# Kernel optimization log

Hardware: AMD Instinct MI355X
Metric: run time of the kernel (lower is better)

The kernel has to match this reference:

```python
import jax, jax.numpy as jnp
import numpy as np

B, N, C = 8, 1024, 768
H = 12
HD = C // H  # 64


def setup_inputs() -> dict:
    key = jax.random.key(0)
    k1, k2, k3, k4 = jax.random.split(key, 4)
    x = jax.random.normal(k1, (B, N, C), dtype=jnp.float32)
    # nn.Linear(dim, 3*dim, bias=False): weight shape [3C, C]
    w_qkv = jax.random.normal(k2, (3 * C, C), dtype=jnp.float32) * (C ** -0.5)
    # nn.Linear(dim, dim): weight [C, C], bias [C]
    w_proj = jax.random.normal(k3, (C, C), dtype=jnp.float32) * (C ** -0.5)
    b_proj = jax.random.normal(k4, (C,), dtype=jnp.float32) * 0.01
    return {"x": x, "w_qkv": w_qkv, "w_proj": w_proj, "b_proj": b_proj}


def reference(x, w_qkv, w_proj, b_proj):
    scale = HD ** -0.5
    qkv = jnp.einsum("bnc,dc->bnd", x, w_qkv)  # [B,N,3C]
    qkv = qkv.reshape(B, N, 3, H, HD).transpose(2, 0, 3, 1, 4)  # [3,B,H,N,HD]
    q, k, v = qkv[0], qkv[1], qkv[2]
    attn = jnp.einsum("bhqd,bhkd->bhqk", q, k) * scale  # [B,H,N,N]
    attn = jax.nn.softmax(attn, axis=-1)
    out = jnp.einsum("bhqk,bhkd->bhqd", attn, v)  # [B,H,N,HD]
    out = out.transpose(0, 2, 1, 3).reshape(B, N, C)
    return jnp.einsum("bnc,dc->bnd", out, w_proj) + b_proj
```

## Files before the change

### kernel.cpp

```cpp
#include <hip/hip_runtime.h>
#include <hip/hip_bf16.h>


typedef __attribute__((ext_vector_type(8))) short bf16x8;
typedef __attribute__((ext_vector_type(4))) float f32x4;
typedef __attribute__((ext_vector_type(4))) short s16x4;

static constexpr int BB  = 8;
static constexpr int SEQ = 1024;
static constexpr int CH  = 768;
static constexpr int NH  = 12;
static constexpr int HD  = 64;
static constexpr int MT  = BB * SEQ;
static constexpr int C3  = 3 * CH;

__device__ __forceinline__ float bf2f(short s) {
    unsigned u = ((unsigned)(unsigned short)s) << 16;
    return __builtin_bit_cast(float, u);
}
__device__ __forceinline__ short f2bf(float f) {
    unsigned u = __builtin_bit_cast(unsigned, f);
    u += 0x7FFF + ((u >> 16) & 1);
    return (short)(u >> 16);
}
__device__ __forceinline__ void async16(const short* g, short* l) {
    __builtin_amdgcn_global_load_lds(
        (const __attribute__((address_space(1))) void*)g,
        (__attribute__((address_space(3))) void*)l, 16, 0, 0);
}

__global__ __launch_bounds__(256) void cvt3(
    const float* __restrict__ a, short* __restrict__ da, int na,
    const float* __restrict__ b, short* __restrict__ db, int nb,
    const float* __restrict__ c, short* __restrict__ dc, int nc)
{
    long i = (long)(blockIdx.x * 256 + threadIdx.x) * 8;
    const float* s; short* d; long off;
    if (i < na)                 { s = a; d = da; off = i; }
    else if (i < (long)na + nb) { s = b; d = db; off = i - na; }
    else                        { s = c; d = dc; off = i - na - nb; }
    float4 x0 = *(const float4*)&s[off];
    float4 x1 = *(const float4*)&s[off + 4];
    bf16x8 o;
    o[0] = f2bf(x0.x); o[1] = f2bf(x0.y); o[2] = f2bf(x0.z); o[3] = f2bf(x0.w);
    o[4] = f2bf(x1.x); o[5] = f2bf(x1.y); o[6] = f2bf(x1.z); o[7] = f2bf(x1.w);
    *(bf16x8*)&d[off] = o;
}

template <bool F32OUT>
__global__ __launch_bounds__(256) void gemm_bt(
    const short* __restrict__ A, const short* __restrict__ Bt,
    const float* __restrict__ bias, void* __restrict__ outp,
    int Ndim, int K)
{
    __shared__ __align__(16) short As[128 * 32];
    __shared__ __align__(16) short Bs[128 * 32];
    const int tid  = threadIdx.x;
    const int wave = tid >> 6, lane = tid & 63;
    const int quad = lane >> 4, l16 = lane & 15;
    const int wr = wave >> 1, wc = wave & 1;
    const int row0 = blockIdx.y * 128, col0 = blockIdx.x * 128;

    f32x4 acc[4][4] = {};

    for (int kb = 0; kb < K; kb += 32) {
        #pragma unroll
        for (int i = 0; i < 2; ++i) {
            int g = i * 256 + wave * 64 + lane;
            int r = g >> 2, cb = (g & 3) * 8;
            async16(&A[(long)(row0 + r) * K + kb + cb], &As[(i * 256 + wave * 64) * 8]);
            async16(&Bt[(long)(col0 + r) * K + kb + cb], &Bs[(i * 256 + wave * 64) * 8]);
        }
        __syncthreads();

        bf16x8 af[4], bfr[4];
        #pragma unroll
        for (int mi = 0; mi < 4; ++mi)
            af[mi] = *(const bf16x8*)&As[(wr * 64 + mi * 16 + l16) * 32 + quad * 8];
        #pragma unroll
        for (int ni = 0; ni < 4; ++ni)
            bfr[ni] = *(const bf16x8*)&Bs[(wc * 64 + ni * 16 + l16) * 32 + quad * 8];
        #pragma unroll
        for (int mi = 0; mi < 4; ++mi)
            #pragma unroll
            for (int ni = 0; ni < 4; ++ni)
                acc[mi][ni] = __builtin_amdgcn_mfma_f32_16x16x32_bf16(
                    af[mi], bfr[ni], acc[mi][ni], 0, 0, 0);
        __syncthreads();
    }

    #pragma unroll
    for (int mi = 0; mi < 4; ++mi) {
        #pragma unroll
        for (int ni = 0; ni < 4; ++ni) {
            int col = col0 + wc * 64 + ni * 16 + l16;
            float bv = bias ? bias[col] : 0.0f;
            #pragma unroll
            for (int r = 0; r < 4; ++r) {
                int row = row0 + wr * 64 + mi * 16 + quad * 4 + r;
                if (F32OUT)
                    ((float*)outp)[(long)row * Ndim + col] = acc[mi][ni][r] + bv;
                else
                    ((short*)outp)[(long)row * Ndim + col] = f2bf(acc[mi][ni][r] + bv);
            }
        }
    }
}

__global__ __launch_bounds__(256, 3) void attn(
    const short* __restrict__ qkv, short* __restrict__ attout)
{
    constexpr int STK = 72, STV = 68, STP = 68;
    __shared__ __align__(16) short Ks [2][64 * STK];
    __shared__ __align__(16) short Vts[2][64 * STV];
    __shared__ __align__(16) short Ps [2][4][16 * STP];
    const int tid  = threadIdx.x;
    const int wave = tid >> 6, lane = tid & 63;
    const int quad = lane >> 4, l16 = lane & 15;
    const int hb = blockIdx.x, h = hb % NH, b = hb / NH;
    const int qbase = blockIdx.y * 128;
    const long base = (long)b * SEQ * C3;
    const int koff = CH + h * HD, voff = 2 * CH + h * HD;

    bf16x8 aq[2][2];
    #pragma unroll
    for (int qt = 0; qt < 2; ++qt) {
        const long qp = base + (long)(qbase + qt * 64 + wave * 16 + l16) * C3 + h * HD;
        aq[qt][0] = *(const bf16x8*)&qkv[qp + quad * 8];
        aq[qt][1] = *(const bf16x8*)&qkv[qp + 32 + quad * 8];
        #pragma unroll
        for (int j = 0; j < 8; ++j) {
            aq[qt][0][j] = f2bf(bf2f(aq[qt][0][j]) * 0.125f);
            aq[qt][1][j] = f2bf(bf2f(aq[qt][1][j]) * 0.125f);
        }
    }

    float lacc[2] = {0.0f, 0.0f};
    f32x4 acc[2][4] = {};

    const int kr = tid >> 3, kc = (tid & 7) * 8;
    const int vr = tid >> 2, vc = (tid & 3) * 16;

    bf16x8 k0r, k1r, v0r, v1r;
    auto gload = [&](int kb) {
        k0r = *(const bf16x8*)&qkv[base + (long)(kb + kr) * C3 + koff + kc];
        k1r = *(const bf16x8*)&qkv[base + (long)(kb + kr + 32) * C3 + koff + kc];
        v0r = *(const bf16x8*)&qkv[base + (long)(kb + vr) * C3 + voff + vc];
        v1r = *(const bf16x8*)&qkv[base + (long)(kb + vr) * C3 + voff + vc + 8];
    };
    gload(0);

    const int nit = SEQ / 64;
    for (int it = 0; it < nit; ++it) {
        const int bufi = it & 1;
        *(bf16x8*)&Ks[bufi][kr * STK + kc]        = k0r;
        *(bf16x8*)&Ks[bufi][(kr + 32) * STK + kc] = k1r;
        #pragma unroll
        for (int j = 0; j < 8; ++j) {
            Vts[bufi][(vc + j) * STV + vr]     = v0r[j];
            Vts[bufi][(vc + 8 + j) * STV + vr] = v1r[j];
        }
        if (it + 1 < nit) gload((it + 1) * 64);
        __syncthreads();
        const short* Kb = Ks[bufi];
        const short* Vb = Vts[bufi];

        #pragma unroll
        for (int qt = 0; qt < 2; ++qt) {
            f32x4 St[4];
            #pragma unroll
            for (int t = 0; t < 4; ++t) {
                bf16x8 k0 = *(const bf16x8*)&Kb[(t * 16 + l16) * STK + quad * 8];
                bf16x8 k1 = *(const bf16x8*)&Kb[(t * 16 + l16) * STK + 32 + quad * 8];
                f32x4 s = {};
                s = __builtin_amdgcn_mfma_f32_16x16x32_bf16(k0, aq[qt][0], s, 0, 0, 0);
                s = __builtin_amdgcn_mfma_f32_16x16x32_bf16(k1, aq[qt][1], s, 0, 0, 0);
                St[t] = s;
            }

            #pragma unroll
            for (int t = 0; t < 4; ++t) {
                float p0 = __expf(St[t][0]), p1 = __expf(St[t][1]);
                float p2 = __expf(St[t][2]), p3 = __expf(St[t][3]);
                lacc[qt] += (p0 + p1) + (p2 + p3);
                s16x4 pk;
                pk[0] = f2bf(p0); pk[1] = f2bf(p1); pk[2] = f2bf(p2); pk[3] = f2bf(p3);
                *(s16x4*)&Ps[qt][wave][l16 * STP + t * 16 + quad * 4] = pk;
            }

            #pragma unroll
            for (int kt = 0; kt < 2; ++kt) {
                bf16x8 pf;
                *(s16x4*)&pf         = *(const s16x4*)&Ps[qt][wave][l16 * STP + kt * 32 + quad * 8];
                *(((s16x4*)&pf) + 1) = *(const s16x4*)&Ps[qt][wave][l16 * STP + kt * 32 + quad * 8 + 4];
                #pragma unroll
                for (int nb = 0; nb < 4; ++nb) {
                    bf16x8 vf;
                    *(s16x4*)&vf         = *(const s16x4*)&Vb[(nb * 16 + l16) * STV + kt * 32 + quad * 8];
                    *(((s16x4*)&vf) + 1) = *(const s16x4*)&Vb[(nb * 16 + l16) * STV + kt * 32 + quad * 8 + 4];
                    acc[qt][nb] = __builtin_amdgcn_mfma_f32_16x16x32_bf16(pf, vf, acc[qt][nb], 0, 0, 0);
                }
            }
        }
    }

    #pragma unroll
    for (int qt = 0; qt < 2; ++qt) {
        float l = lacc[qt];
        l += __shfl_xor(l, 16);
        l += __shfl_xor(l, 32);
        #pragma unroll
        for (int r = 0; r < 4; ++r) {
            float linv = 1.0f / __shfl(l, quad * 4 + r);
            int row = qbase + qt * 64 + wave * 16 + quad * 4 + r;
            #pragma unroll
            for (int nb = 0; nb < 4; ++nb)
                attout[((long)b * SEQ + row) * CH + h * HD + nb * 16 + l16] =
                    f2bf(acc[qt][nb][r] * linv);
        }
    }
}

extern "C" void kernel_launch(void* const* d_in, const int* in_sizes, int n_in,
                              void* d_out, int out_size, void* d_ws, size_t ws_size,
                              hipStream_t stream) {
    const float* x      = (const float*)d_in[0];
    const float* w_qkv  = (const float*)d_in[1];
    const float* w_proj = (const float*)d_in[2];
    const float* b_proj = (const float*)d_in[3];

    const int nx = MT * CH, nq = C3 * CH, np = CH * CH;

    short* xb      = (short*)d_ws;
    short* wqkvb   = xb + nx;
    short* wprojb  = wqkvb + nq;
    short* qkv     = wprojb + np;
    short* attnout = xb;

    cvt3<<<(nx + nq + np) / 2048, 256, 0, stream>>>(
        x, xb, nx, w_qkv, wqkvb, nq, w_proj, wprojb, np);

    gemm_bt<false><<<dim3(C3 / 128, MT / 128), 256, 0, stream>>>(
        xb, wqkvb, nullptr, qkv, C3, CH);
    attn<<<dim3(96, 8), 256, 0, stream>>>(qkv, attnout);
    gemm_bt<true><<<dim3(CH / 128, MT / 128), 256, 0, stream>>>(
        attnout, wprojb, b_proj, (float*)d_out, CH, CH);
}
```

Before: 214.2 us.

## Widen GEMM K-tile to 64, compute softmax row sums via MFMA, simplify attention loads

The GEMM now stages 64-wide K slices per barrier pair, which halves the number of syncs, and raises the launch-bounds occupancy hint to 4. In attention, the softmax denominator is computed by an extra MFMA against a ones vector instead of scalar adds and shuffles. The P staging buffer is shared across both query tiles, and bf16 packing uses a cheaper round-half-up perm. V loads are remapped so each lane reads its own row, and pointers are incremented instead of recomputed. These changes cost extra LDS in the GEMM and slightly different rounding of P.

```diff
diff --git a/kernel.cpp b/kernel.cpp
--- a/kernel.cpp
+++ b/kernel.cpp
@@ -22,6 +22,11 @@
     unsigned u = __builtin_bit_cast(unsigned, f);
     u += 0x7FFF + ((u >> 16) & 1);
     return (short)(u >> 16);
+}
+__device__ __forceinline__ unsigned pack_bf2(float lo, float hi) {
+    unsigned ul = __builtin_bit_cast(unsigned, lo) + 0x8000u;
+    unsigned uh = __builtin_bit_cast(unsigned, hi) + 0x8000u;
+    return __builtin_amdgcn_perm(uh, ul, 0x07060302);
 }
 __device__ __forceinline__ void async16(const short* g, short* l) {
     __builtin_amdgcn_global_load_lds(
@@ -48,13 +53,13 @@
 }
 
 template <bool F32OUT>
-__global__ __launch_bounds__(256) void gemm_bt(
+__global__ __launch_bounds__(256, 4) void gemm_bt(
     const short* __restrict__ A, const short* __restrict__ Bt,
     const float* __restrict__ bias, void* __restrict__ outp,
     int Ndim, int K)
 {
-    __shared__ __align__(16) short As[128 * 32];
-    __shared__ __align__(16) short Bs[128 * 32];
+    __shared__ __align__(16) short As[128 * 64];
+    __shared__ __align__(16) short Bs[128 * 64];
     const int tid  = threadIdx.x;
     const int wave = tid >> 6, lane = tid & 63;
     const int quad = lane >> 4, l16 = lane & 15;
@@ -63,29 +68,32 @@
 
     f32x4 acc[4][4] = {};
 
-    for (int kb = 0; kb < K; kb += 32) {
-        #pragma unroll
-        for (int i = 0; i < 2; ++i) {
-            int g = i * 256 + wave * 64 + lane;
-            int r = g >> 2, cb = (g & 3) * 8;
-            async16(&A[(long)(row0 + r) * K + kb + cb], &As[(i * 256 + wave * 64) * 8]);
-            async16(&Bt[(long)(col0 + r) * K + kb + cb], &Bs[(i * 256 + wave * 64) * 8]);
+    for (int kb = 0; kb < K; kb += 64) {
+        #pragma unroll
+        for (int p = 0; p < 4; ++p) {
+            int g = p * 256 + wave * 64 + lane;
+            int r = g >> 3, cb = (g & 7) * 8;
+            async16(&A[(long)(row0 + r) * K + kb + cb], &As[(p * 256 + wave * 64) * 8]);
+            async16(&Bt[(long)(col0 + r) * K + kb + cb], &Bs[(p * 256 + wave * 64) * 8]);
         }
         __syncthreads();
 
-        bf16x8 af[4], bfr[4];
-        #pragma unroll
-        for (int mi = 0; mi < 4; ++mi)
-            af[mi] = *(const bf16x8*)&As[(wr * 64 + mi * 16 + l16) * 32 + quad * 8];
-        #pragma unroll
-        for (int ni = 0; ni < 4; ++ni)
-            bfr[ni] = *(const bf16x8*)&Bs[(wc * 64 + ni * 16 + l16) * 32 + quad * 8];
-        #pragma unroll
-        for (int mi = 0; mi < 4; ++mi)
+        #pragma unroll
+        for (int kh = 0; kh < 2; ++kh) {
+            bf16x8 af[4], bfr[4];
+            #pragma unroll
+            for (int mi = 0; mi < 4; ++mi)
+                af[mi] = *(const bf16x8*)&As[(wr * 64 + mi * 16 + l16) * 64 + kh * 32 + quad * 8];
             #pragma unroll
             for (int ni = 0; ni < 4; ++ni)
-                acc[mi][ni] = __builtin_amdgcn_mfma_f32_16x16x32_bf16(
-                    af[mi], bfr[ni], acc[mi][ni], 0, 0, 0);
+                bfr[ni] = *(const bf16x8*)&Bs[(wc * 64 + ni * 16 + l16) * 64 + kh * 32 + quad * 8];
+            #pragma unroll
+            for (int mi = 0; mi < 4; ++mi)
+                #pragma unroll
+                for (int ni = 0; ni < 4; ++ni)
+                    acc[mi][ni] = __builtin_amdgcn_mfma_f32_16x16x32_bf16(
+                        af[mi], bfr[ni], acc[mi][ni], 0, 0, 0);
+        }
         __syncthreads();
     }
 
@@ -113,14 +121,13 @@
     constexpr int STK = 72, STV = 68, STP = 68;
     __shared__ __align__(16) short Ks [2][64 * STK];
     __shared__ __align__(16) short Vts[2][64 * STV];
-    __shared__ __align__(16) short Ps [2][4][16 * STP];
+    __shared__ __align__(16) short Ps [4][16 * STP];
     const int tid  = threadIdx.x;
     const int wave = tid >> 6, lane = tid & 63;
     const int quad = lane >> 4, l16 = lane & 15;
     const int hb = blockIdx.x, h = hb % NH, b = hb / NH;
     const int qbase = blockIdx.y * 128;
     const long base = (long)b * SEQ * C3;
-    const int koff = CH + h * HD, voff = 2 * CH + h * HD;
 
     bf16x8 aq[2][2];
     #pragma unroll
@@ -135,20 +142,23 @@
         }
     }
 
-    float lacc[2] = {0.0f, 0.0f};
+    bf16x8 onesv;
+    #pragma unroll
+    for (int j = 0; j < 8; ++j) onesv[j] = (short)0x3F80;
+
     f32x4 acc[2][4] = {};
+    f32x4 accl[2] = {};
 
     const int kr = tid >> 3, kc = (tid & 7) * 8;
-    const int vr = tid >> 2, vc = (tid & 3) * 16;
+    const short* kp0 = qkv + base + (long)kr * C3 + (CH + h * HD) + kc;
+    const short* kp1 = kp0 + (long)32 * C3;
+    const short* vp  = qkv + base + (long)lane * C3 + (2 * CH + h * HD) + wave * 16;
 
     bf16x8 k0r, k1r, v0r, v1r;
-    auto gload = [&](int kb) {
-        k0r = *(const bf16x8*)&qkv[base + (long)(kb + kr) * C3 + koff + kc];
-        k1r = *(const bf16x8*)&qkv[base + (long)(kb + kr + 32) * C3 + koff + kc];
-        v0r = *(const bf16x8*)&qkv[base + (long)(kb + vr) * C3 + voff + vc];
-        v1r = *(const bf16x8*)&qkv[base + (long)(kb + vr) * C3 + voff + vc + 8];
-    };
-    gload(0);
+    k0r = *(const bf16x8*)kp0;
+    k1r = *(const bf16x8*)kp1;
+    v0r = *(const bf16x8*)vp;
+    v1r = *(const bf16x8*)(vp + 8);
 
     const int nit = SEQ / 64;
     for (int it = 0; it < nit; ++it) {
@@ -157,10 +167,16 @@
         *(bf16x8*)&Ks[bufi][(kr + 32) * STK + kc] = k1r;
         #pragma unroll
         for (int j = 0; j < 8; ++j) {
-            Vts[bufi][(vc + j) * STV + vr]     = v0r[j];
-            Vts[bufi][(vc + 8 + j) * STV + vr] = v1r[j];
-        }
-        if (it + 1 < nit) gload((it + 1) * 64);
+            Vts[bufi][(wave * 16 + j) * STV + lane]     = v0r[j];
+            Vts[bufi][(wave * 16 + 8 + j) * STV + lane] = v1r[j];
+        }
+        if (it + 1 < nit) {
+            kp0 += (long)64 * C3; kp1 += (long)64 * C3; vp += (long)64 * C3;
+            k0r = *(const bf16x8*)kp0;
+            k1r = *(const bf16x8*)kp1;
+            v0r = *(const bf16x8*)vp;
+            v1r = *(const bf16x8*)(vp + 8);
+        }
         __syncthreads();
         const short* Kb = Ks[bufi];
         const short* Vb = Vts[bufi];
@@ -180,19 +196,18 @@
 
             #pragma unroll
             for (int t = 0; t < 4; ++t) {
-                float p0 = __expf(St[t][0]), p1 = __expf(St[t][1]);
-                float p2 = __expf(St[t][2]), p3 = __expf(St[t][3]);
-                lacc[qt] += (p0 + p1) + (p2 + p3);
-                s16x4 pk;
-                pk[0] = f2bf(p0); pk[1] = f2bf(p1); pk[2] = f2bf(p2); pk[3] = f2bf(p3);
-                *(s16x4*)&Ps[qt][wave][l16 * STP + t * 16 + quad * 4] = pk;
+                unsigned w0 = pack_bf2(__expf(St[t][0]), __expf(St[t][1]));
+                unsigned w1 = pack_bf2(__expf(St[t][2]), __expf(St[t][3]));
+                uint2 pk; pk.x = w0; pk.y = w1;
+                *(uint2*)&Ps[wave][l16 * STP + t * 16 + quad * 4] = pk;
             }
 
             #pragma unroll
             for (int kt = 0; kt < 2; ++kt) {
                 bf16x8 pf;
-                *(s16x4*)&pf         = *(const s16x4*)&Ps[qt][wave][l16 * STP + kt * 32 + quad * 8];
-                *(((s16x4*)&pf) + 1) = *(const s16x4*)&Ps[qt][wave][l16 * STP + kt * 32 + quad * 8 + 4];
+                *(s16x4*)&pf         = *(const s16x4*)&Ps[wave][l16 * STP + kt * 32 + quad * 8];
+                *(((s16x4*)&pf) + 1) = *(const s16x4*)&Ps[wave][l16 * STP + kt * 32 + quad * 8 + 4];
+                accl[qt] = __builtin_amdgcn_mfma_f32_16x16x32_bf16(pf, onesv, accl[qt], 0, 0, 0);
                 #pragma unroll
                 for (int nb = 0; nb < 4; ++nb) {
                     bf16x8 vf;
@@ -206,12 +221,9 @@
 
     #pragma unroll
     for (int qt = 0; qt < 2; ++qt) {
-        float l = lacc[qt];
-        l += __shfl_xor(l, 16);
-        l += __shfl_xor(l, 32);
         #pragma unroll
         for (int r = 0; r < 4; ++r) {
-            float linv = 1.0f / __shfl(l, quad * 4 + r);
+            float linv = 1.0f / accl[qt][r];
             int row = qbase + qt * 64 + wave * 16 + quad * 4 + r;
             #pragma unroll
             for (int nb = 0; nb < 4; ++nb)
```

Result: faster. 207.6 us (-3.1%).
